# Performance work log

Hardware: AMD Instinct MI355X
Metric: run time of the kernel (lower is better)

## Reference

```python
import jax, jax.numpy as jnp
import numpy as np

NEG_SLOPE = 0.2
BN_EPS = 1e-5


def _gatv2(x, Wl, Wr, att, b, src, dst, N):
    # PyG GATv2Conv, concat=False: lin_l on source, lin_r on target,
    # e = a^T LeakyReLU(x_l[j] + x_r[i]); softmax over incoming edges of i;
    # out = mean_h( sum_j alpha_ij * x_l[j] ) + bias
    H, C = att.shape
    xl = (x @ Wl).reshape(N, H, C)
    xr = (x @ Wr).reshape(N, H, C)
    e = jax.nn.leaky_relu(xl[src] + xr[dst], NEG_SLOPE)          # [E,H,C]
    score = jnp.einsum('ehc,hc->eh', e, att)                     # [E,H]
    m = jax.ops.segment_max(score, dst, num_segments=N)          # [N,H]
    a = jnp.exp(score - m[dst])
    denom = jax.ops.segment_sum(a, dst, num_segments=N)
    alpha = a / denom[dst]                                       # [E,H]
    out = jax.ops.segment_sum(alpha[..., None] * xl[src], dst, num_segments=N)  # [N,H,C]
    return out.mean(axis=1) + b


def _bn(h, g, be):
    # BatchNorm1d, training-mode statistics (biased variance)
    mu = h.mean(axis=0)
    var = h.var(axis=0)
    return g * (h - mu) * jax.lax.rsqrt(var + BN_EPS) + be


def _gelu(x):
    return jax.nn.gelu(x, approximate=False)


def setup_inputs() -> dict:
    key = jax.random.key(0)
    N, F, HID, LAT, H, E, G = 50000, 64, 64, 64, 4, 800000, 256
    ks = jax.random.split(key, 32)
    d = {}
    d['x'] = jax.random.normal(ks[0], (N, F), dtype=jnp.float32)
    d['edge_src'] = jax.random.randint(ks[1], (E,), 0, N, dtype=jnp.int32)
    d['edge_dst'] = jax.random.randint(ks[2], (E,), 0, N, dtype=jnp.int32)
    d['batch'] = jnp.sort(jax.random.randint(ks[3], (N,), 0, G, dtype=jnp.int32))
    d['num_graphs'] = G
    def lin(k, fi, fo):
        return jax.random.normal(k, (fi, fo), dtype=jnp.float32) / np.sqrt(fi)
    i = 4
    for L, fin in zip((1, 2, 3), (F, HID, HID)):
        d[f'Wl{L}'] = lin(ks[i], fin, H * HID); i += 1
        d[f'Wr{L}'] = lin(ks[i], fin, H * HID); i += 1
        d[f'att{L}'] = jax.random.normal(ks[i], (H, HID), dtype=jnp.float32) / np.sqrt(HID); i += 1
        d[f'b{L}'] = jnp.zeros((HID,), dtype=jnp.float32)
        d[f'g{L}'] = jax.random.uniform(ks[i], (HID,), dtype=jnp.float32, minval=0.5, maxval=1.5); i += 1
        d[f'be{L}'] = 0.1 * jax.random.normal(ks[i], (HID,), dtype=jnp.float32); i += 1
    d['Wmu'] = lin(ks[i], HID, LAT); i += 1
    d['bmu'] = jnp.zeros((LAT,), dtype=jnp.float32)
    d['Wlv'] = lin(ks[i], HID, LAT); i += 1
    d['blv'] = jnp.zeros((LAT,), dtype=jnp.float32)
    return d


def reference(x, edge_src, edge_dst, batch, num_graphs,
              Wl1, Wr1, att1, b1, g1, be1,
              Wl2, Wr2, att2, b2, g2, be2,
              Wl3, Wr3, att3, b3, g3, be3,
              Wmu, bmu, Wlv, blv):
    N = x.shape[0]
    loops = jnp.arange(N, dtype=edge_src.dtype)
    src = jnp.concatenate([edge_src, loops])  # add_self_loops=True (PyG default)
    dst = jnp.concatenate([edge_dst, loops])

    h = _gelu(_bn(_gatv2(x, Wl1, Wr1, att1, b1, src, dst, N), g1, be1))
    h_in = h
    h = _gelu(_bn(_gatv2(h, Wl2, Wr2, att2, b2, src, dst, N), g2, be2)) + h_in
    h_in = h
    h = _gelu(_bn(_gatv2(h, Wl3, Wr3, att3, b3, src, dst, N), g3, be3)) + h_in

    h_pool = jax.ops.segment_sum(h, batch, num_segments=num_graphs)  # global_add_pool
    return (h_pool @ Wmu + bmu, h_pool @ Wlv + blv)
```

## Files before the change

### kernel.cpp

```cpp
#include <hip/hip_runtime.h>
#include <math.h>

typedef __attribute__((ext_vector_type(8))) short bf16x8;
typedef __attribute__((ext_vector_type(4))) float f32x4;
typedef __attribute__((ext_vector_type(2))) float f32x2;

static __device__ __forceinline__ unsigned short f2bf(float f) {
  unsigned u = __float_as_uint(f);
  unsigned r = (u + 0x7FFF + ((u >> 16) & 1)) >> 16;
  return (unsigned short)r;
}
static __device__ __forceinline__ float bf2f(unsigned short b) {
  return __uint_as_float(((unsigned)b) << 16);
}

#define DPP_ADD(x, ctrl) \
  ((x) + __int_as_float(__builtin_amdgcn_update_dpp(0, __float_as_int(x), (ctrl), 0xf, 0xf, false)))

#define NSHARD 64
#define NEB 256


__global__ __launch_bounds__(256) void k_prep(const float* __restrict__ W0, const float* __restrict__ W1,
                                              const float* __restrict__ W2, const float* __restrict__ W3,
                                              const float* __restrict__ W4, const float* __restrict__ W5,
                                              unsigned short* __restrict__ wt,
                                              const int* __restrict__ edst,
                                              int* __restrict__ bktcnt, int E, int N) {
  if (blockIdx.x < 384) {
    int gid = blockIdx.x * 256 + threadIdx.x;
    int m = gid >> 14;
    int r = gid & 16383;
    int k = r >> 8;
    int n = r & 255;
    const float* W = (m == 0) ? W0 : (m == 1) ? W1 : (m == 2) ? W2
                   : (m == 3) ? W3 : (m == 4) ? W4 : W5;
    wt[(size_t)m * 16384 + n * 64 + k] = f2bf(W[k * 256 + n]);
    return;
  }
  const int b = blockIdx.x - 384;
  if (b >= NEB) return;
  const int nbk = (N + 255) >> 8;
  __shared__ int h[256];
  h[threadIdx.x] = 0;
  __syncthreads();
  const int chunk = (E + NEB - 1) / NEB;
  const int e0 = b * chunk, e1 = min(e0 + chunk, E);
  for (int e = e0 + threadIdx.x; e < e1; e += 256) atomicAdd(&h[edst[e] >> 8], 1);
  __syncthreads();
  if (threadIdx.x < nbk && h[threadIdx.x]) atomicAdd(&bktcnt[threadIdx.x], h[threadIdx.x]);
}


__global__ __launch_bounds__(256) void k_bscan(const int* __restrict__ bktcnt,
                                               int* __restrict__ bktptr,
                                               int* __restrict__ bktcur,
                                               int* __restrict__ rowptr,
                                               int* __restrict__ colb, int N, int E) {
  const int nbk = (N + 255) >> 8;
  __shared__ int s[256];
  int v = (threadIdx.x < nbk) ? bktcnt[threadIdx.x] : 0;
  s[threadIdx.x] = v;
  __syncthreads();
  for (int off = 1; off < 256; off <<= 1) {
    int t = (threadIdx.x >= off) ? s[threadIdx.x - off] : 0;
    __syncthreads();
    s[threadIdx.x] += t;
    __syncthreads();
  }
  int ex = s[threadIdx.x] - v;
  if (threadIdx.x < nbk) {
    bktptr[threadIdx.x] = ex;
    bktcur[threadIdx.x] = ex;
  }
  if (threadIdx.x == 0) { bktptr[nbk] = E; rowptr[N] = E; }
  if (threadIdx.x < 16) colb[E + threadIdx.x] = 0;
}


__global__ __launch_bounds__(256) void k_place(const int* __restrict__ esrc,
                                               const int* __restrict__ edst,
                                               int* __restrict__ bktcur,
                                               int2* __restrict__ ebuf, int E, int N) {
  const int nbk = (N + 255) >> 8;
  __shared__ int cnt[256], base[256];
  cnt[threadIdx.x] = 0;
  __syncthreads();
  const int chunk = (E + NEB - 1) / NEB;
  const int e0 = blockIdx.x * chunk, e1 = min(e0 + chunk, E);
  for (int e = e0 + threadIdx.x; e < e1; e += 256) atomicAdd(&cnt[edst[e] >> 8], 1);
  __syncthreads();
  if (threadIdx.x < nbk && cnt[threadIdx.x])
    base[threadIdx.x] = atomicAdd(&bktcur[threadIdx.x], cnt[threadIdx.x]);
  cnt[threadIdx.x] = 0;
  __syncthreads();
  for (int e = e0 + threadIdx.x; e < e1; e += 256) {
    int d = edst[e];
    int bk = d >> 8;
    int p = base[bk] + atomicAdd(&cnt[bk], 1);
    ebuf[p] = make_int2(d, esrc[e]);
  }
}


static __device__ __forceinline__ void csr_pass2(const int2* __restrict__ ebuf,
                                                 const int* __restrict__ bktptr,
                                                 int* __restrict__ rowptr,
                                                 int* __restrict__ colb,
                                                 int N, char* smem) {
  const int b = blockIdx.x;
  const int nbk = (N + 255) >> 8;
  if (b >= nbk) return;
  int* hist = (int*)smem;
  int* s = (int*)smem + 256;
  const int tid = threadIdx.x;
  const int lo = bktptr[b], hi = bktptr[b + 1];
  hist[tid] = 0;
  __syncthreads();
  for (int i = lo + tid; i < hi; i += 256) atomicAdd(&hist[ebuf[i].x & 255], 1);
  __syncthreads();
  int v = hist[tid];
  s[tid] = v;
  __syncthreads();
  for (int off = 1; off < 256; off <<= 1) {
    int t = (tid >= off) ? s[tid - off] : 0;
    __syncthreads();
    s[tid] += t;
    __syncthreads();
  }
  int pos = lo + s[tid] - v;
  int node = (b << 8) + tid;
  if (node < N) rowptr[node] = pos;
  hist[tid] = pos;
  __syncthreads();
  for (int i = lo + tid; i < hi; i += 256) {
    int2 e = ebuf[i];
    int p = atomicAdd(&hist[e.x & 255], 1);
    colb[p] = e.y << 9;
  }
}


static __device__ __forceinline__ void mm_gemm(const float* __restrict__ src,
                                               const float* __restrict__ bnsums,
                                               const float* __restrict__ g,
                                               const float* __restrict__ be,
                                               const float* __restrict__ resid,
                                               float* __restrict__ hout,
                                               const unsigned short* __restrict__ wt,
                                               unsigned short* __restrict__ xlb,
                                               unsigned short* __restrict__ xrb,
                                               int N, int ntiles, float inv_n,
                                               char* smem) {
  unsigned short* Bs = (unsigned short*)smem;
  unsigned short* Ah = (unsigned short*)(smem + 32768);
  unsigned short* Al = (unsigned short*)(smem + 36864);
  const int t = threadIdx.x;
  const unsigned short* wb = wt + (blockIdx.y ? 16384 : 0);
  unsigned short* dst = blockIdx.y ? xrb : xlb;

  const int wave = t >> 6, lane = t & 63;
  const int rw = (wave & 1) * 16, cw = (wave >> 1) * 128;
  const int m15 = lane & 15, quad = lane >> 4;
  const int arow = t >> 3, ac0 = (t & 7) * 8;
  const int aoff = arow * 64 + (((t & 7) ^ (arow & 7)) << 3);

  float scale[8], shift[8];
  if (bnsums) {
    float* stat = (float*)smem;
    if (t < 128) {
      float a = 0.f;
#pragma unroll
      for (int sd = 0; sd < NSHARD; ++sd) a += bnsums[sd * 128 + t];
      stat[t] = a;
    }
    __syncthreads();
#pragma unroll
    for (int i = 0; i < 8; ++i) {
      int c = ac0 + i;
      float mu = stat[c] * inv_n;
      float var = stat[64 + c] * inv_n - mu * mu;
      float rs = rsqrtf(var + 1e-5f) * g[c];
      scale[i] = rs;
      shift[i] = be[c] - mu * rs;
    }
    __syncthreads();
  }

#pragma unroll
  for (int j = 0; j < 8; ++j) {
    int cidx = t + 256 * j;
    int n = cidx >> 3, gg = cidx & 7;
    *(bf16x8*)&Bs[n * 64 + (((gg ^ ((n >> 3) & 7))) << 3)] =
        *(const bf16x8*)(wb + (size_t)n * 64 + gg * 8);
  }

  const bool wr_h = (hout != nullptr) && (blockIdx.y == 0);
  const int gstride = gridDim.x;

  float4 a0, a1, rv0, rv1;
  auto loadA = [&](int tl, float4& x0, float4& x1, float4& r0v, float4& r1v) {
    x0 = make_float4(0.f, 0.f, 0.f, 0.f);
    x1 = make_float4(0.f, 0.f, 0.f, 0.f);
    r0v = make_float4(0.f, 0.f, 0.f, 0.f);
    r1v = make_float4(0.f, 0.f, 0.f, 0.f);
    int gr = tl * 32 + arow;
    if (tl < ntiles && gr < N) {
      x0 = *(const float4*)(src + (size_t)gr * 64 + ac0);
      x1 = *(const float4*)(src + (size_t)gr * 64 + ac0 + 4);
      if (resid) {
        r0v = *(const float4*)(resid + (size_t)gr * 64 + ac0);
        r1v = *(const float4*)(resid + (size_t)gr * 64 + ac0 + 4);
      }
    }
  };
  loadA(blockIdx.x, a0, a1, rv0, rv1);

  for (int tile = blockIdx.x; tile < ntiles; tile += gstride) {
    int r0 = tile * 32;
    int gr = r0 + arow;
    {
      float vs[8] = {a0.x, a0.y, a0.z, a0.w, a1.x, a1.y, a1.z, a1.w};
      if (bnsums) {
        float rv[8] = {rv0.x, rv0.y, rv0.z, rv0.w, rv1.x, rv1.y, rv1.z, rv1.w};
#pragma unroll
        for (int i = 0; i < 8; ++i) {
          float v = fmaf(vs[i], scale[i], shift[i]);
          float ge = 0.5f * v * (1.f + erff(v * 0.70710678118654752f));
          vs[i] = ge + rv[i];
        }
        if (wr_h && gr < N) {
          float4 o0 = {vs[0], vs[1], vs[2], vs[3]};
          float4 o1 = {vs[4], vs[5], vs[6], vs[7]};
          *(float4*)(hout + (size_t)gr * 64 + ac0) = o0;
          *(float4*)(hout + (size_t)gr * 64 + ac0 + 4) = o1;
        }
      }
      bf16x8 hi8, lo8;
#pragma unroll
      for (int i = 0; i < 8; ++i) {
        unsigned short hh = f2bf(vs[i]);
        hi8[i] = (short)hh;
        lo8[i] = (short)f2bf(vs[i] - bf2f(hh));
      }
      *(bf16x8*)&Ah[aoff] = hi8;
      *(bf16x8*)&Al[aoff] = lo8;
    }
    __syncthreads();

    loadA(tile + gstride, a0, a1, rv0, rv1);

    f32x4 acc[8];
#pragma unroll
    for (int s = 0; s < 8; ++s) acc[s] = (f32x4){0.f, 0.f, 0.f, 0.f};
    const int xq = m15 & 7;
#pragma unroll
    for (int kk = 0; kk < 64; kk += 32) {
      const int ga = (((kk >> 3) + quad) ^ xq) << 3;
      bf16x8 ah = *(const bf16x8*)&Ah[(rw + m15) * 64 + ga];
      bf16x8 al = *(const bf16x8*)&Al[(rw + m15) * 64 + ga];
#pragma unroll
      for (int s = 0; s < 8; ++s) {
        bf16x8 b = *(const bf16x8*)&Bs[(cw + m15 * 8 + s) * 64 + ga];
        acc[s] = __builtin_amdgcn_mfma_f32_16x16x32_bf16(ah, b, acc[s], 0, 0, 0);
        acc[s] = __builtin_amdgcn_mfma_f32_16x16x32_bf16(al, b, acc[s], 0, 0, 0);
      }
    }
#pragma unroll
    for (int r = 0; r < 4; ++r) {
      int row_g = r0 + rw + quad * 4 + r;
      if (row_g < N) {
        bf16x8 o;
#pragma unroll
        for (int s = 0; s < 8; ++s) o[s] = (short)f2bf(acc[s][r]);
        *(bf16x8*)(dst + (size_t)row_g * 256 + cw + m15 * 8) = o;
      }
    }
    __syncthreads();
  }
}

__global__ __launch_bounds__(256, 4) void k_mm0(const float* __restrict__ src,
                                                const unsigned short* __restrict__ wt,
                                                unsigned short* __restrict__ xlb,
                                                unsigned short* __restrict__ xrb,
                                                const int2* __restrict__ ebuf,
                                                const int* __restrict__ bktptr,
                                                int* __restrict__ rowptr,
                                                int* __restrict__ colb,
                                                int N, int ntiles) {
  __shared__ __align__(16) char smem[40960];
  if (blockIdx.y == 2) {
    csr_pass2(ebuf, bktptr, rowptr, colb, N, smem);
    return;
  }
  mm_gemm(src, nullptr, nullptr, nullptr, nullptr, nullptr, wt, xlb, xrb, N, ntiles, 0.f, smem);
}

__global__ __launch_bounds__(256, 4) void k_mm1(const float* __restrict__ src,
                                                const float* __restrict__ bnsums,
                                                const float* __restrict__ g,
                                                const float* __restrict__ be,
                                                float* __restrict__ hout,
                                                const unsigned short* __restrict__ wt,
                                                unsigned short* __restrict__ xlb,
                                                unsigned short* __restrict__ xrb,
                                                int N, int ntiles, float inv_n) {
  __shared__ __align__(16) char smem[40960];
  mm_gemm(src, bnsums, g, be, nullptr, hout, wt, xlb, xrb, N, ntiles, inv_n, smem);
}

__global__ __launch_bounds__(256, 4) void k_mm2(const float* __restrict__ src,
                                                const float* __restrict__ bnsums,
                                                const float* __restrict__ g,
                                                const float* __restrict__ be,
                                                const float* __restrict__ resid,
                                                float* __restrict__ hout,
                                                const unsigned short* __restrict__ wt,
                                                unsigned short* __restrict__ xlb,
                                                unsigned short* __restrict__ xrb,
                                                int N, int ntiles, float inv_n) {
  __shared__ __align__(16) char smem[40960];
  mm_gemm(src, bnsums, g, be, resid, hout, wt, xlb, xrb, N, ntiles, inv_n, smem);
}


static __device__ __forceinline__ void gat_body(const unsigned short* __restrict__ xlb,
                                                const unsigned short* __restrict__ xrb,
                                                const float* __restrict__ att,
                                                const float* __restrict__ bias,
                                                const int* __restrict__ rowptr,
                                                const int* __restrict__ colb,
                                                float* __restrict__ out,
                                                float* __restrict__ bnsums, int N) {
  __shared__ float sres[4][64];
  const int lane = threadIdx.x & 63;
  const int wv = threadIdx.x >> 6;
  const int node0 = blockIdx.x * 4 + wv;
  const bool valid = node0 < N;
  const int node = __builtin_amdgcn_readfirstlane(valid ? node0 : 0);
  const int beg = rowptr[node];
  const int end = valid ? rowptr[node + 1] : beg;

  const char* base = (const char*)xlb + (size_t)lane * 8;
  int o0 = colb[beg], o1 = colb[beg + 1], o2 = colb[beg + 2], o3 = colb[beg + 3];
  uint2 vbs = *(const uint2*)(base + (size_t)(unsigned)(node << 9));
  uint2 d0 = *(const uint2*)(base + (size_t)(unsigned)o0);
  uint2 d1 = *(const uint2*)(base + (size_t)(unsigned)o1);
  uint2 d2 = *(const uint2*)(base + (size_t)(unsigned)o2);
  uint2 d3 = *(const uint2*)(base + (size_t)(unsigned)o3);
  int p0 = colb[beg + 4], p1 = colb[beg + 5], p2 = colb[beg + 6], p3 = colb[beg + 7];
  uint2 t0 = *(const uint2*)(base + (size_t)(unsigned)p0);
  uint2 t1 = *(const uint2*)(base + (size_t)(unsigned)p1);
  uint2 t2 = *(const uint2*)(base + (size_t)(unsigned)p2);
  uint2 t3 = *(const uint2*)(base + (size_t)(unsigned)p3);
  int f0 = colb[beg + 8], f1 = colb[beg + 9], f2 = colb[beg + 10], f3 = colb[beg + 11];

  float4 a4 = *(const float4*)(att + lane * 4);
  const float LOG2E = 1.4426950408889634f;
  const f32x2 a01 = {a4.x * LOG2E, a4.y * LOG2E};
  const f32x2 a23 = {a4.z * LOG2E, a4.w * LOG2E};
  const f32x2 c02 = {0.2f, 0.2f};
  uint2 xru = *(const uint2*)((const char*)xrb + ((size_t)(unsigned)(node << 9)) + lane * 8);
  const f32x2 xr01 = {__uint_as_float(xru.x << 16), __uint_as_float(xru.x & 0xFFFF0000u)};
  const f32x2 xr23 = {__uint_as_float(xru.y << 16), __uint_as_float(xru.y & 0xFFFF0000u)};

  f32x2 sv01 = {__uint_as_float(vbs.x << 16), __uint_as_float(vbs.x & 0xFFFF0000u)};
  f32x2 sv23 = {__uint_as_float(vbs.y << 16), __uint_as_float(vbs.y & 0xFFFF0000u)};
  float m;
  {
    f32x2 s01 = sv01 + xr01;
    f32x2 s23 = sv23 + xr23;
    s01 = __builtin_elementwise_max(s01, s01 * c02);
    s23 = __builtin_elementwise_max(s23, s23 * c02);
    f32x2 q = __builtin_elementwise_fma(s23, a23, s01 * a01);
    float p = q.x + q.y;
    p = DPP_ADD(p, 0xB1);
    p = DPP_ADD(p, 0x4E);
    p = DPP_ADD(p, 0x124);
    p = DPP_ADD(p, 0x128);
    m = p;
  }
  float lsum = 1.f;
  f32x2 o01 = sv01, o23 = sv23;

  auto proc = [&](uint2 vb, bool ok) {
    f32x2 v01 = {__uint_as_float(vb.x << 16), __uint_as_float(vb.x & 0xFFFF0000u)};
    f32x2 v23 = {__uint_as_float(vb.y << 16), __uint_as_float(vb.y & 0xFFFF0000u)};
    f32x2 s01 = v01 + xr01;
    f32x2 s23 = v23 + xr23;
    s01 = __builtin_elementwise_max(s01, s01 * c02);
    s23 = __builtin_elementwise_max(s23, s23 * c02);
    f32x2 q = __builtin_elementwise_fma(s23, a23, s01 * a01);
    float p = q.x + q.y;
    p = DPP_ADD(p, 0xB1);
    p = DPP_ADD(p, 0x4E);
    p = DPP_ADD(p, 0x124);
    p = DPP_ADD(p, 0x128);
    float w = __builtin_amdgcn_exp2f(fminf(p - m, 126.f));
    w = ok ? w : 0.f;
    lsum += w;
    f32x2 w2 = {w, w};
    o01 = __builtin_elementwise_fma(w2, v01, o01);
    o23 = __builtin_elementwise_fma(w2, v23, o23);
  };

  for (int e = beg; e < end; e += 4) {
    uint2 u0 = *(const uint2*)(base + (size_t)(unsigned)f0);
    uint2 u1 = *(const uint2*)(base + (size_t)(unsigned)f1);
    uint2 u2 = *(const uint2*)(base + (size_t)(unsigned)f2);
    uint2 u3 = *(const uint2*)(base + (size_t)(unsigned)f3);
    f0 = colb[e + 12]; f1 = colb[e + 13]; f2 = colb[e + 14]; f3 = colb[e + 15];
    proc(d0, true);
    proc(d1, e + 1 < end);
    proc(d2, e + 2 < end);
    proc(d3, e + 3 < end);
    d0 = t0; d1 = t1; d2 = t2; d3 = t3;
    t0 = u0; t1 = u1; t2 = u2; t3 = u3;
  }

  float inv = __builtin_amdgcn_rcpf(lsum);
  float rx = o01.x * inv, ry = o01.y * inv, rz = o23.x * inv, rw2 = o23.y * inv;
  rx += __shfl_xor(rx, 16, 64); rx += __shfl_xor(rx, 32, 64);
  ry += __shfl_xor(ry, 16, 64); ry += __shfl_xor(ry, 32, 64);
  rz += __shfl_xor(rz, 16, 64); rz += __shfl_xor(rz, 32, 64);
  rw2 += __shfl_xor(rw2, 16, 64); rw2 += __shfl_xor(rw2, 32, 64);
  if (lane < 16) {
    float4 res = {0.f, 0.f, 0.f, 0.f};
    if (valid) {
      float4 b4 = *(const float4*)(bias + lane * 4);
      res.x = 0.25f * rx + b4.x;
      res.y = 0.25f * ry + b4.y;
      res.z = 0.25f * rz + b4.z;
      res.w = 0.25f * rw2 + b4.w;
      *(float4*)(out + (size_t)node * 64 + lane * 4) = res;
    }
    *(float4*)&sres[wv][lane * 4] = res;
  }
  __syncthreads();
  if (threadIdx.x < 64) {
    int c = threadIdx.x;
    float s0 = sres[0][c], s1 = sres[1][c], s2 = sres[2][c], s3 = sres[3][c];
    float* bs = bnsums + (size_t)(blockIdx.x & (NSHARD - 1)) * 128;
    atomicAdd(&bs[c], s0 + s1 + s2 + s3);
    atomicAdd(&bs[64 + c], s0 * s0 + s1 * s1 + s2 * s2 + s3 * s3);
  }
}

__global__ __launch_bounds__(256) void k_gat0(const unsigned short* __restrict__ xlb,
                                              const unsigned short* __restrict__ xrb,
                                              const float* __restrict__ att,
                                              const float* __restrict__ bias,
                                              const int* __restrict__ rowptr,
                                              const int* __restrict__ colb,
                                              float* __restrict__ out,
                                              float* __restrict__ bnsums, int N) {
  gat_body(xlb, xrb, att, bias, rowptr, colb, out, bnsums, N);
}
__global__ __launch_bounds__(256) void k_gat1(const unsigned short* __restrict__ xlb,
                                              const unsigned short* __restrict__ xrb,
                                              const float* __restrict__ att,
                                              const float* __restrict__ bias,
                                              const int* __restrict__ rowptr,
                                              const int* __restrict__ colb,
                                              float* __restrict__ out,
                                              float* __restrict__ bnsums, int N) {
  gat_body(xlb, xrb, att, bias, rowptr, colb, out, bnsums, N);
}
__global__ __launch_bounds__(256) void k_gat2(const unsigned short* __restrict__ xlb,
                                              const unsigned short* __restrict__ xrb,
                                              const float* __restrict__ att,
                                              const float* __restrict__ bias,
                                              const int* __restrict__ rowptr,
                                              const int* __restrict__ colb,
                                              float* __restrict__ out,
                                              float* __restrict__ bnsums, int N) {
  gat_body(xlb, xrb, att, bias, rowptr, colb, out, bnsums, N);
}


__global__ __launch_bounds__(256) void k_bn_pool(const float* __restrict__ gat,
                                                 const float* __restrict__ bnsums,
                                                 const float* __restrict__ g,
                                                 const float* __restrict__ be,
                                                 const float* __restrict__ resid,
                                                 const int* __restrict__ batch,
                                                 float* __restrict__ pool,
                                                 int N, float inv_n) {
  __shared__ float sc[64], sh[64];
  if (threadIdx.x < 64) {
    int c = threadIdx.x;
    float s = 0.f, q = 0.f;
    for (int sd = 0; sd < NSHARD; ++sd) {
      s += bnsums[sd * 128 + c];
      q += bnsums[sd * 128 + 64 + c];
    }
    float mu = s * inv_n;
    float var = q * inv_n - mu * mu;
    float rs = rsqrtf(var + 1e-5f) * g[c];
    sc[c] = rs;
    sh[c] = be[c] - mu * rs;
  }
  __syncthreads();
  const int c = threadIdx.x & 63;
  const int wv = threadIdx.x >> 6;
  int n0 = (blockIdx.x * 4 + wv) * 32;
  if (n0 >= N) return;
  int n1 = min(n0 + 32, N);
  int curg = batch[n0];
  float acc = 0.f;
  for (int n = n0; n < n1; ++n) {
    int b = batch[n];
    if (b != curg) {
      atomicAdd(&pool[(size_t)curg * 64 + c], acc);
      acc = 0.f;
      curg = b;
    }
    float v = fmaf(gat[(size_t)n * 64 + c], sc[c], sh[c]);
    float ge = 0.5f * v * (1.f + erff(v * 0.70710678118654752f));
    acc += ge + resid[(size_t)n * 64 + c];
  }
  atomicAdd(&pool[(size_t)curg * 64 + c], acc);
}


__global__ void k_head(const float* __restrict__ pool, const float* __restrict__ Wmu,
                       const float* __restrict__ bmu, const float* __restrict__ Wlv,
                       const float* __restrict__ blv, float* __restrict__ out, int G) {
  int g = blockIdx.x;
  int c = threadIdx.x;
  __shared__ float row[64];
  row[c] = pool[(size_t)g * 64 + c];
  __syncthreads();
  float am = 0.f, al = 0.f;
  for (int k = 0; k < 64; ++k) {
    float r = row[k];
    am = fmaf(r, Wmu[k * 64 + c], am);
    al = fmaf(r, Wlv[k * 64 + c], al);
  }
  out[(size_t)g * 64 + c] = am + bmu[c];
  out[(size_t)G * 64 + (size_t)g * 64 + c] = al + blv[c];
}


extern "C" void kernel_launch(void* const* d_in, const int* in_sizes, int n_in,
                              void* d_out, int out_size, void* d_ws, size_t ws_size,
                              hipStream_t stream) {
  const float* x    = (const float*)d_in[0];
  const int* esrc   = (const int*)d_in[1];
  const int* edst   = (const int*)d_in[2];
  const int* batch  = (const int*)d_in[3];
  const float* Wl[3]  = {(const float*)d_in[5],  (const float*)d_in[11], (const float*)d_in[17]};
  const float* Wr[3]  = {(const float*)d_in[6],  (const float*)d_in[12], (const float*)d_in[18]};
  const float* att[3] = {(const float*)d_in[7],  (const float*)d_in[13], (const float*)d_in[19]};
  const float* bia[3] = {(const float*)d_in[8],  (const float*)d_in[14], (const float*)d_in[20]};
  const float* gam[3] = {(const float*)d_in[9],  (const float*)d_in[15], (const float*)d_in[21]};
  const float* bet[3] = {(const float*)d_in[10], (const float*)d_in[16], (const float*)d_in[22]};
  const float* Wmu = (const float*)d_in[23];
  const float* bmu = (const float*)d_in[24];
  const float* Wlv = (const float*)d_in[25];
  const float* blv = (const float*)d_in[26];
  float* out = (float*)d_out;

  const int N = in_sizes[0] / 64;
  const int E = in_sizes[1];
  const int G = out_size / 128;

  char* p = (char*)d_ws;
  auto alloc = [&](size_t bytes) -> void* {
    void* r = (void*)p;
    p += (bytes + 255) & ~(size_t)255;
    return r;
  };
  int*   bktcnt  = (int*)alloc(256 * 4);
  float* bnsums  = (float*)alloc(3 * NSHARD * 128 * 4);
  float* pool    = (float*)alloc((size_t)G * 64 * 4);
  char*  zend    = p;
  unsigned short* xlb = (unsigned short*)alloc((size_t)N * 256 * 2);
  unsigned short* xrb = (unsigned short*)alloc((size_t)N * 256 * 2);
  float* hA     = (float*)alloc((size_t)N * 64 * 4);
  float* hB     = (float*)alloc((size_t)N * 64 * 4);
  float* gat    = (float*)alloc((size_t)N * 64 * 4);
  int*   rowptr = (int*)alloc((size_t)(N + 1) * 4);
  int*   bktptr = (int*)alloc(260 * 4);
  int*   bktcur = (int*)alloc(256 * 4);
  int*   colb   = (int*)alloc((size_t)(E + 16) * 4);
  int2*  ebuf   = (int2*)alloc((size_t)E * 8);
  unsigned short* wt = (unsigned short*)alloc(6 * 16384 * 2);

  const int nbGat = (N + 3) / 4;
  const int ntiles = (N + 31) / 32;
  const float inv_n = 1.f / (float)N;

  hipMemsetAsync(bktcnt, 0, (size_t)(zend - (char*)bktcnt), stream);

  k_prep<<<384 + NEB, 256, 0, stream>>>(Wl[0], Wr[0], Wl[1], Wr[1], Wl[2], Wr[2], wt,
                                        edst, bktcnt, E, N);
  k_bscan<<<1, 256, 0, stream>>>(bktcnt, bktptr, bktcur, rowptr, colb, N, E);
  k_place<<<NEB, 256, 0, stream>>>(esrc, edst, bktcur, ebuf, E, N);

  float* bns0 = bnsums;
  float* bns1 = bnsums + NSHARD * 128;
  float* bns2 = bnsums + 2 * NSHARD * 128;

  k_mm0<<<dim3(512, 3), 256, 0, stream>>>(x, wt, xlb, xrb, ebuf, bktptr, rowptr, colb,
                                          N, ntiles);
  k_gat0<<<nbGat, 256, 0, stream>>>(xlb, xrb, att[0], bia[0], rowptr, colb, gat, bns0, N);
  k_mm1<<<dim3(512, 2), 256, 0, stream>>>(gat, bns0, gam[0], bet[0], hA,
                                          wt + 2 * 16384, xlb, xrb, N, ntiles, inv_n);
  k_gat1<<<nbGat, 256, 0, stream>>>(xlb, xrb, att[1], bia[1], rowptr, colb, gat, bns1, N);
  k_mm2<<<dim3(512, 2), 256, 0, stream>>>(gat, bns1, gam[1], bet[1], hA, hB,
                                          wt + 4 * 16384, xlb, xrb, N, ntiles, inv_n);
  k_gat2<<<nbGat, 256, 0, stream>>>(xlb, xrb, att[2], bia[2], rowptr, colb, gat, bns2, N);
  k_bn_pool<<<(N + 127) / 128, 256, 0, stream>>>(gat, bns2, gam[2], bet[2], hB, batch, pool,
                                                 N, inv_n);
  k_head<<<G, 64, 0, stream>>>(pool, Wmu, bmu, Wlv, blv, out, G);
}
```

Before: 420.6 us.

## Pad CSR rows to multiples of four and pack degree into rowptr for vector index loads

Each node's neighbour list now starts at a 4-aligned offset, claimed through a global atomic cursor, and the degree is packed into the upper bits of rowptr. The GAT kernel can then read the column indices as aligned int4 loads and needs only one rowptr read per node instead of two. The colb buffer grows by up to 3N entries and is zeroed by the memset so the padding is safe, and the DPP bound_ctrl flag is also flipped. The risks are that positions must stay below 2^22 and degree below 1024, and that blocks now claim their output ranges in nondeterministic order.

Result: no change. 420.1 us (-0.1%).

```diff
diff --git a/kernel.cpp b/kernel.cpp
--- a/kernel.cpp
+++ b/kernel.cpp
@@ -15,7 +15,7 @@
 }
 
 #define DPP_ADD(x, ctrl) \
-  ((x) + __int_as_float(__builtin_amdgcn_update_dpp(0, __float_as_int(x), (ctrl), 0xf, 0xf, false)))
+  ((x) + __int_as_float(__builtin_amdgcn_update_dpp(0, __float_as_int(x), (ctrl), 0xf, 0xf, true)))
 
 #define NSHARD 64
 #define NEB 256
@@ -55,8 +55,7 @@
 __global__ __launch_bounds__(256) void k_bscan(const int* __restrict__ bktcnt,
                                                int* __restrict__ bktptr,
                                                int* __restrict__ bktcur,
-                                               int* __restrict__ rowptr,
-                                               int* __restrict__ colb, int N, int E) {
+                                               int N, int E) {
   const int nbk = (N + 255) >> 8;
   __shared__ int s[256];
   int v = (threadIdx.x < nbk) ? bktcnt[threadIdx.x] : 0;
@@ -73,8 +72,7 @@
     bktptr[threadIdx.x] = ex;
     bktcur[threadIdx.x] = ex;
   }
-  if (threadIdx.x == 0) { bktptr[nbk] = E; rowptr[N] = E; }
-  if (threadIdx.x < 16) colb[E + threadIdx.x] = 0;
+  if (threadIdx.x == 0) bktptr[nbk] = E;
 }
 
 
@@ -107,20 +105,23 @@
                                                  const int* __restrict__ bktptr,
                                                  int* __restrict__ rowptr,
                                                  int* __restrict__ colb,
+                                                 int* __restrict__ ccur,
                                                  int N, char* smem) {
   const int b = blockIdx.x;
   const int nbk = (N + 255) >> 8;
   if (b >= nbk) return;
   int* hist = (int*)smem;
   int* s = (int*)smem + 256;
+  int* sb = (int*)smem + 512;
   const int tid = threadIdx.x;
   const int lo = bktptr[b], hi = bktptr[b + 1];
   hist[tid] = 0;
   __syncthreads();
   for (int i = lo + tid; i < hi; i += 256) atomicAdd(&hist[ebuf[i].x & 255], 1);
   __syncthreads();
-  int v = hist[tid];
-  s[tid] = v;
+  int deg = hist[tid];
+  int pd = (deg + 3) & ~3;
+  s[tid] = pd;
   __syncthreads();
   for (int off = 1; off < 256; off <<= 1) {
     int t = (tid >= off) ? s[tid - off] : 0;
@@ -128,9 +129,11 @@
     s[tid] += t;
     __syncthreads();
   }
-  int pos = lo + s[tid] - v;
+  if (tid == 255) sb[0] = atomicAdd(ccur, s[255]);
+  __syncthreads();
+  int pos = sb[0] + s[tid] - pd;
   int node = (b << 8) + tid;
-  if (node < N) rowptr[node] = pos;
+  if (node < N) rowptr[node] = (int)((unsigned)pos | ((unsigned)deg << 22));
   hist[tid] = pos;
   __syncthreads();
   for (int i = lo + tid; i < hi; i += 256) {
@@ -288,10 +291,11 @@
                                                 const int* __restrict__ bktptr,
                                                 int* __restrict__ rowptr,
                                                 int* __restrict__ colb,
+                                                int* __restrict__ ccur,
                                                 int N, int ntiles) {
   __shared__ __align__(16) char smem[40960];
   if (blockIdx.y == 2) {
-    csr_pass2(ebuf, bktptr, rowptr, colb, N, smem);
+    csr_pass2(ebuf, bktptr, rowptr, colb, ccur, N, smem);
     return;
   }
   mm_gemm(src, nullptr, nullptr, nullptr, nullptr, nullptr, wt, xlb, xrb, N, ntiles, 0.f, smem);
@@ -339,29 +343,33 @@
   const int node0 = blockIdx.x * 4 + wv;
   const bool valid = node0 < N;
   const int node = __builtin_amdgcn_readfirstlane(valid ? node0 : 0);
-  const int beg = rowptr[node];
-  const int end = valid ? rowptr[node + 1] : beg;
-
-  const char* base = (const char*)xlb + (size_t)lane * 8;
-  int o0 = colb[beg], o1 = colb[beg + 1], o2 = colb[beg + 2], o3 = colb[beg + 3];
-  uint2 vbs = *(const uint2*)(base + (size_t)(unsigned)(node << 9));
-  uint2 d0 = *(const uint2*)(base + (size_t)(unsigned)o0);
-  uint2 d1 = *(const uint2*)(base + (size_t)(unsigned)o1);
-  uint2 d2 = *(const uint2*)(base + (size_t)(unsigned)o2);
-  uint2 d3 = *(const uint2*)(base + (size_t)(unsigned)o3);
-  int p0 = colb[beg + 4], p1 = colb[beg + 5], p2 = colb[beg + 6], p3 = colb[beg + 7];
-  uint2 t0 = *(const uint2*)(base + (size_t)(unsigned)p0);
-  uint2 t1 = *(const uint2*)(base + (size_t)(unsigned)p1);
-  uint2 t2 = *(const uint2*)(base + (size_t)(unsigned)p2);
-  uint2 t3 = *(const uint2*)(base + (size_t)(unsigned)p3);
-  int f0 = colb[beg + 8], f1 = colb[beg + 9], f2 = colb[beg + 10], f3 = colb[beg + 11];
+  const int rp = rowptr[node];
+  const int beg = rp & 0x3FFFFF;
+  const int deg = (int)(((unsigned)rp) >> 22);
+  const int end = valid ? beg + deg : beg;
+
+  const char* xl = (const char*)xlb;
+  const unsigned lb = (unsigned)lane * 8u;
+
+  int4 c0 = *(const int4*)(colb + beg);
+  int4 c1 = *(const int4*)(colb + beg + 4);
+  uint2 vbs = *(const uint2*)(xl + ((unsigned)(node << 9) + lb));
+  uint2 d0 = *(const uint2*)(xl + ((unsigned)c0.x + lb));
+  uint2 d1 = *(const uint2*)(xl + ((unsigned)c0.y + lb));
+  uint2 d2 = *(const uint2*)(xl + ((unsigned)c0.z + lb));
+  uint2 d3 = *(const uint2*)(xl + ((unsigned)c0.w + lb));
+  uint2 t0 = *(const uint2*)(xl + ((unsigned)c1.x + lb));
+  uint2 t1 = *(const uint2*)(xl + ((unsigned)c1.y + lb));
+  uint2 t2 = *(const uint2*)(xl + ((unsigned)c1.z + lb));
+  uint2 t3 = *(const uint2*)(xl + ((unsigned)c1.w + lb));
+  int4 cn = *(const int4*)(colb + beg + 8);
 
   float4 a4 = *(const float4*)(att + lane * 4);
   const float LOG2E = 1.4426950408889634f;
   const f32x2 a01 = {a4.x * LOG2E, a4.y * LOG2E};
   const f32x2 a23 = {a4.z * LOG2E, a4.w * LOG2E};
   const f32x2 c02 = {0.2f, 0.2f};
-  uint2 xru = *(const uint2*)((const char*)xrb + ((size_t)(unsigned)(node << 9)) + lane * 8);
+  uint2 xru = *(const uint2*)((const char*)xrb + ((unsigned)(node << 9) + lb));
   const f32x2 xr01 = {__uint_as_float(xru.x << 16), __uint_as_float(xru.x & 0xFFFF0000u)};
   const f32x2 xr23 = {__uint_as_float(xru.y << 16), __uint_as_float(xru.y & 0xFFFF0000u)};
 
@@ -406,11 +414,11 @@
   };
 
   for (int e = beg; e < end; e += 4) {
-    uint2 u0 = *(const uint2*)(base + (size_t)(unsigned)f0);
-    uint2 u1 = *(const uint2*)(base + (size_t)(unsigned)f1);
-    uint2 u2 = *(const uint2*)(base + (size_t)(unsigned)f2);
-    uint2 u3 = *(const uint2*)(base + (size_t)(unsigned)f3);
-    f0 = colb[e + 12]; f1 = colb[e + 13]; f2 = colb[e + 14]; f3 = colb[e + 15];
+    uint2 u0 = *(const uint2*)(xl + ((unsigned)cn.x + lb));
+    uint2 u1 = *(const uint2*)(xl + ((unsigned)cn.y + lb));
+    uint2 u2 = *(const uint2*)(xl + ((unsigned)cn.z + lb));
+    uint2 u3 = *(const uint2*)(xl + ((unsigned)cn.w + lb));
+    cn = *(const int4*)(colb + e + 12);
     proc(d0, true);
     proc(d1, e + 1 < end);
     proc(d2, e + 2 < end);
@@ -575,6 +583,8 @@
   int*   bktcnt  = (int*)alloc(256 * 4);
   float* bnsums  = (float*)alloc(3 * NSHARD * 128 * 4);
   float* pool    = (float*)alloc((size_t)G * 64 * 4);
+  int*   ccur    = (int*)alloc(256);
+  int*   colb    = (int*)alloc(((size_t)E + 3 * (size_t)N + 64) * 4);
   char*  zend    = p;
   unsigned short* xlb = (unsigned short*)alloc((size_t)N * 256 * 2);
   unsigned short* xrb = (unsigned short*)alloc((size_t)N * 256 * 2);
@@ -584,7 +594,6 @@
   int*   rowptr = (int*)alloc((size_t)(N + 1) * 4);
   int*   bktptr = (int*)alloc(260 * 4);
   int*   bktcur = (int*)alloc(256 * 4);
-  int*   colb   = (int*)alloc((size_t)(E + 16) * 4);
   int2*  ebuf   = (int2*)alloc((size_t)E * 8);
   unsigned short* wt = (unsigned short*)alloc(6 * 16384 * 2);
 
@@ -596,7 +605,7 @@
 
   k_prep<<<384 + NEB, 256, 0, stream>>>(Wl[0], Wr[0], Wl[1], Wr[1], Wl[2], Wr[2], wt,
                                         edst, bktcnt, E, N);
-  k_bscan<<<1, 256, 0, stream>>>(bktcnt, bktptr, bktcur, rowptr, colb, N, E);
+  k_bscan<<<1, 256, 0, stream>>>(bktcnt, bktptr, bktcur, N, E);
   k_place<<<NEB, 256, 0, stream>>>(esrc, edst, bktcur, ebuf, E, N);
 
   float* bns0 = bnsums;
@@ -604,7 +613,7 @@
   float* bns2 = bnsums + 2 * NSHARD * 128;
 
   k_mm0<<<dim3(512, 3), 256, 0, stream>>>(x, wt, xlb, xrb, ebuf, bktptr, rowptr, colb,
-                                          N, ntiles);
+                                          ccur, N, ntiles);
   k_gat0<<<nbGat, 256, 0, stream>>>(xlb, xrb, att[0], bia[0], rowptr, colb, gat, bns0, N);
   k_mm1<<<dim3(512, 2), 256, 0, stream>>>(gat, bns0, gam[0], bet[0], hA,
                                           wt + 2 * 16384, xlb, xrb, N, ntiles, inv_n);
```
